# Optimization experiments

Hardware: AMD Instinct MI355X
Metric: run time of the kernel (lower is better)

## Reference

```python
import jax, jax.numpy as jnp
import numpy as np

B, T, D = 2, 4096, 512
H, W = 8, 32
HD = D // H            # 64
HIDDEN = 3 * D         # SwiGLU expansion = 3
SCALE = float(np.sqrt(HD))
EPS = 1e-5


def setup_inputs() -> dict:
    key = jax.random.key(0)
    ks = jax.random.split(key, 8)
    s = 0.02  # small init for weight matrices
    return {
        "x": jax.random.normal(ks[0], (B, T, D), dtype=jnp.float32),
        "pre_g": jnp.ones((D,), jnp.float32), "pre_b": jnp.zeros((D,), jnp.float32),
        "wq": jax.random.normal(ks[1], (D, D), jnp.float32) * s,
        "wkv": jax.random.normal(ks[2], (D, 2 * D), jnp.float32) * s,
        "wo": jax.random.normal(ks[3], (D, D), jnp.float32) * s,
        "attn_g": jnp.ones((D,), jnp.float32), "attn_b": jnp.zeros((D,), jnp.float32),
        "freqs": jax.random.normal(ks[4], (D,), jnp.float32) * 0.02,
        "phases": jnp.zeros((D,), jnp.float32),
        "amp": jnp.full((1,), 0.1, jnp.float32),
        "w_gate": jax.random.normal(ks[5], (D, HIDDEN), jnp.float32) * s,
        "w_val": jax.random.normal(ks[6], (D, HIDDEN), jnp.float32) * s,
        "w_proj": jax.random.normal(ks[7], (HIDDEN, D), jnp.float32) * s,
        "ffn_g": jnp.ones((D,), jnp.float32), "ffn_b": jnp.zeros((D,), jnp.float32),
    }


def _ln(x, g, b):
    mu = jnp.mean(x, axis=-1, keepdims=True)
    var = jnp.mean(jnp.square(x - mu), axis=-1, keepdims=True)
    return (x - mu) * jax.lax.rsqrt(var + EPS) * g + b


def _gather_window(z):
    # z: (B, T, H, C) -> nb: (B, T, W, H, C) with nb[:, t, w] = z[:, t-1-w] (zeros if t-1-w < 0)
    zp = jnp.pad(z, ((0, 0), (W, 0), (0, 0), (0, 0)))
    idx = jnp.arange(T)[:, None] + (W - 1) - jnp.arange(W)[None, :]  # (T, W), values in [0, T+W-1)
    return zp[:, idx]  # (B, T, W, H, C)


def reference(x, pre_g, pre_b, wq, wkv, wo, attn_g, attn_b,
              freqs, phases, amp, w_gate, w_val, w_proj, ffn_g, ffn_b):
    h = _ln(x, pre_g, pre_b)

    # ---- multi-head causal tension (sigmoid local attention) ----
    q = (h @ wq).reshape(B, T, H, HD)
    kv = (h @ wkv).reshape(B, T, H, 2 * HD)
    nb_kv = _gather_window(kv)                     # (B, T, W, H, 2*HD)
    nb_k, nb_v = nb_kv[..., :HD], nb_kv[..., HD:]
    tau = jax.nn.sigmoid(jnp.einsum('bthd,btwhd->bthw', q, nb_k) / SCALE)
    msg = jnp.einsum('bthw,btwhd->bthd', tau, nb_v).reshape(B, T, D)
    h = _ln(h + msg @ wo, attn_g, attn_b)

    # ---- oscillatory modulation ----
    pos = jnp.arange(T, dtype=jnp.float32)[:, None]  # (T, 1)
    mod = jnp.sin(pos * freqs + phases)              # (T, D)
    y = h * (1.0 + amp * mod)[None]

    # ---- SwiGLU FFN ----
    z = (jax.nn.silu(y @ w_gate) * (y @ w_val)) @ w_proj
    return _ln(y + z, ffn_g, ffn_b)
```

## Files before the change

kernel.cpp:

```cpp
#include <hip/hip_runtime.h>
#include <hip/hip_bf16.h>
#include <math.h>

#define T_LEN   4096
#define D_DIM   512
#define H_NUM   8
#define HD_DIM  64
#define W_WIN   32
#define HID_DIM 1536
#define M_ROWS  8192
#define QKV_LD  1536
#define BK 64

typedef __hip_bfloat16 bf16;
typedef __bf16  bf16x8 __attribute__((ext_vector_type(8)));
typedef __bf16  bf16x4 __attribute__((ext_vector_type(4)));
typedef float   f32x4  __attribute__((ext_vector_type(4)));

#define G_AS __attribute__((address_space(1)))
#define L_AS __attribute__((address_space(3)))

#define SBAR()        __builtin_amdgcn_s_barrier()
#define SCHED_FENCE() __builtin_amdgcn_sched_barrier(0)
#define WAIT_VM(N)    asm volatile("s_waitcnt vmcnt(" #N ")" ::: "memory")
#define WAIT_LGKM0()  asm volatile("s_waitcnt lgkmcnt(0)" ::: "memory")

__device__ __forceinline__ float b2f(bf16 x) { return __bfloat162float(x); }
__device__ __forceinline__ bf16  f2b(float x){ return __float2bfloat16(x); }

__device__ __forceinline__ void gload_lds16(const bf16* g, bf16* l) {
  __builtin_amdgcn_global_load_lds((const G_AS unsigned int*)g,
                                   (L_AS unsigned int*)l, 16, 0, 0);
}

__device__ __forceinline__ float rdP(const void* p, int i, bool f32) {
  return f32 ? ((const float*)p)[i] : b2f(((const bf16*)p)[i]);
}

__device__ __forceinline__ float wave_reduce_sum(float v) {
  #pragma unroll
  for (int off = 32; off; off >>= 1) v += __shfl_xor(v, off, 64);
  return v;
}

__device__ __forceinline__ bool detect_f32(const unsigned* __restrict__ x) {
  int lane = threadIdx.x & 63;
  int votes = 0;
  #pragma unroll
  for (int i = 0; i < 4; ++i) {
    unsigned e = (x[lane * 4 + i] >> 7) & 0xffu;
    votes += (e >= 90u && e <= 140u) ? 1 : 0;
  }
  float v = wave_reduce_sum((float)votes);
  return v < 200.f;
}

__device__ __forceinline__ void swizzle_xy(int gx, int& bx, int& by) {
  int lid = blockIdx.x;
  int sub = lid & 7;
  int grp = lid >> 3;
  bx = grp % gx;
  by = (grp / gx) * 8 + sub;
}

__global__ __launch_bounds__(256) void ln_kernel(
    const void* __restrict__ in, const void* __restrict__ g, const void* __restrict__ bb,
    void* __restrict__ out, int mode,
    const void* __restrict__ freqs, const void* __restrict__ phases,
    const void* __restrict__ amp,
    const unsigned* __restrict__ xdet, int in_follows, int out_follows)
{
  bool f32  = detect_f32(xdet);
  bool inF  = f32 && (in_follows != 0);
  bool outF = f32 && (out_follows != 0);

  int wave = threadIdx.x >> 6;
  int lane = threadIdx.x & 63;
  int row  = blockIdx.x * 4 + wave;

  float x[8];
  if (inF) {
    const float* rp = (const float*)in + (size_t)row * D_DIM + lane * 8;
    float4 v0 = *reinterpret_cast<const float4*>(rp);
    float4 v1 = *reinterpret_cast<const float4*>(rp + 4);
    x[0]=v0.x; x[1]=v0.y; x[2]=v0.z; x[3]=v0.w;
    x[4]=v1.x; x[5]=v1.y; x[6]=v1.z; x[7]=v1.w;
  } else {
    bf16x8 v = *reinterpret_cast<const bf16x8*>(
        (const bf16*)in + (size_t)row * D_DIM + lane * 8);
    #pragma unroll
    for (int i = 0; i < 8; ++i) x[i] = (float)v[i];
  }

  float s = 0.f, s2 = 0.f;
  #pragma unroll
  for (int i = 0; i < 8; ++i) { s += x[i]; s2 += x[i]*x[i]; }
  s  = wave_reduce_sum(s);
  s2 = wave_reduce_sum(s2);
  float mu   = s * (1.f / D_DIM);
  float var  = s2 * (1.f / D_DIM) - mu * mu;
  float rstd = rsqrtf(var + 1e-5f);

  int t = row & (T_LEN - 1);
  float ampf = (mode == 1) ? rdP(amp, 0, f32) : 0.f;

  float o[8];
  #pragma unroll
  for (int i = 0; i < 8; ++i) {
    int d = lane * 8 + i;
    float val = (x[i] - mu) * rstd * rdP(g, d, f32) + rdP(bb, d, f32);
    if (mode == 1) {
      float m = __sinf(fmaf((float)t, rdP(freqs, d, f32), rdP(phases, d, f32)));
      val *= (1.f + ampf * m);
    }
    o[i] = val;
  }

  if (outF) {
    float* op = (float*)out + (size_t)row * D_DIM + lane * 8;
    *reinterpret_cast<float4*>(op)     = make_float4(o[0], o[1], o[2], o[3]);
    *reinterpret_cast<float4*>(op + 4) = make_float4(o[4], o[5], o[6], o[7]);
  } else {
    bf16x8 ov;
    #pragma unroll
    for (int i = 0; i < 8; ++i) ov[i] = (__bf16)o[i];
    *reinterpret_cast<bf16x8*>((bf16*)out + (size_t)row * D_DIM + lane * 8) = ov;
  }
}

__global__ __launch_bounds__(256) void prep_kernel(
    const void* s0, const void* s1, const void* s2, const void* s3,
    const void* s4, const void* s5,
    bf16* d0, bf16* d1, bf16* d2, bf16* d3, bf16* d4, bf16* d5,
    const void* __restrict__ xin, const void* __restrict__ pre_g,
    const void* __restrict__ pre_b, bf16* __restrict__ hout,
    const unsigned* __restrict__ xdet)
{
  __shared__ float ftile[32][33];
  bool f32 = detect_f32(xdet);
  int bid = blockIdx.x;

  if (bid >= 3328) {
    int wave = threadIdx.x >> 6;
    int lane = threadIdx.x & 63;
    int row  = (bid - 3328) * 4 + wave;

    float x[8];
    if (f32) {
      const float* rp = (const float*)xin + (size_t)row * D_DIM + lane * 8;
      float4 v0 = *reinterpret_cast<const float4*>(rp);
      float4 v1 = *reinterpret_cast<const float4*>(rp + 4);
      x[0]=v0.x; x[1]=v0.y; x[2]=v0.z; x[3]=v0.w;
      x[4]=v1.x; x[5]=v1.y; x[6]=v1.z; x[7]=v1.w;
    } else {
      bf16x8 v = *reinterpret_cast<const bf16x8*>(
          (const bf16*)xin + (size_t)row * D_DIM + lane * 8);
      #pragma unroll
      for (int i = 0; i < 8; ++i) x[i] = (float)v[i];
    }

    float s = 0.f, s2 = 0.f;
    #pragma unroll
    for (int i = 0; i < 8; ++i) { s += x[i]; s2 += x[i]*x[i]; }
    s  = wave_reduce_sum(s);
    s2 = wave_reduce_sum(s2);
    float mu   = s * (1.f / D_DIM);
    float var  = s2 * (1.f / D_DIM) - mu * mu;
    float rstd = rsqrtf(var + 1e-5f);

    bf16x8 ov;
    #pragma unroll
    for (int i = 0; i < 8; ++i) {
      int d = lane * 8 + i;
      ov[i] = (__bf16)((x[i] - mu) * rstd * rdP(pre_g, d, f32) + rdP(pre_b, d, f32));
    }
    *reinterpret_cast<bf16x8*>(hout + (size_t)row * D_DIM + lane * 8) = ov;
    return;
  }

  const void* src; bf16* dst; int R, C, lid, tiles_x;
  if      (bid < 256)  { src=s0; dst=d0; R=512;  C=512;  lid=bid;      tiles_x=16; }
  else if (bid < 768)  { src=s1; dst=d1; R=512;  C=1024; lid=bid-256;  tiles_x=32; }
  else if (bid < 1024) { src=s2; dst=d2; R=512;  C=512;  lid=bid-768;  tiles_x=16; }
  else if (bid < 1792) { src=s3; dst=d3; R=512;  C=1536; lid=bid-1024; tiles_x=48; }
  else if (bid < 2560) { src=s4; dst=d4; R=512;  C=1536; lid=bid-1792; tiles_x=48; }
  else                 { src=s5; dst=d5; R=1536; C=512;  lid=bid-2560; tiles_x=16; }

  int c0 = (lid % tiles_x) * 32;
  int r0 = (lid / tiles_x) * 32;

  {
    int row = threadIdx.x >> 3;
    int c4  = (threadIdx.x & 7) * 4;
    if (f32) {
      float4 v = *reinterpret_cast<const float4*>(
          (const float*)src + (size_t)(r0 + row) * C + c0 + c4);
      ftile[row][c4]     = v.x;
      ftile[row][c4 + 1] = v.y;
      ftile[row][c4 + 2] = v.z;
      ftile[row][c4 + 3] = v.w;
    } else {
      bf16x4 v = *reinterpret_cast<const bf16x4*>(
          (const bf16*)src + (size_t)(r0 + row) * C + c0 + c4);
      #pragma unroll
      for (int i = 0; i < 4; ++i) ftile[row][c4 + i] = (float)v[i];
    }
  }
  __syncthreads();
  {
    int c  = threadIdx.x >> 3;
    int r4 = (threadIdx.x & 7) * 4;
    bf16x4 ov;
    #pragma unroll
    for (int i = 0; i < 4; ++i) ov[i] = (__bf16)ftile[r4 + i][c];
    *reinterpret_cast<bf16x4*>(dst + (size_t)(c0 + c) * R + r0 + r4) = ov;
  }
}

template<int BNT, bool DBUF>
__global__ __launch_bounds__(512) void gemm_tile_kernel(
    const bf16* __restrict__ A, const bf16* __restrict__ Bt,
    bf16* Cout, const bf16* extra, int N, int K, int lda, int mode, int gx)
{
  constexpr int MI  = (BNT == 128) ? 4 : 2;
  constexpr int NJ  = 2;
  constexpr int NB  = DBUF ? 2 : 1;
  constexpr int ASZ = 128 * BK;
  constexpr int BSZ = BNT * BK;
  constexpr int CPF = 68;
  constexpr int CPB = 136;
  constexpr size_t STAGE = (size_t)NB * (ASZ + BSZ) * 2;
  constexpr size_t CTSZ  = (BNT == 64) ? (size_t)128 * CPF * 4 : (size_t)128 * CPB * 2;
  constexpr size_t SMEMSZ = STAGE > CTSZ ? STAGE : CTSZ;
  __shared__ alignas(16) char smem[SMEMSZ];
  bf16* Asb = (bf16*)smem;
  bf16* Bsb = Asb + (size_t)NB * ASZ;

  int bx, by; swizzle_xy(gx, bx, by);
  int mbase = by * 128, nbase = bx * BNT;
  int tid  = threadIdx.x;
  int lane = tid & 63;
  int wid  = tid >> 6;
  int quad = lane >> 4, l16 = lane & 15;
  int wm, wn;
  if constexpr (BNT == 128) { wm = (wid >> 2) * 64; wn = (wid & 3) * 32; }
  else                      { wm = (wid >> 1) * 32; wn = (wid & 1) * 32; }

  int srow  = tid >> 3;
  int scolb = ((tid & 7) ^ (srow & 7)) * 8;
  const bf16* Ag = A  + (size_t)(mbase + srow) * lda + scolb;
  const bf16* Bg = Bt + (size_t)(nbase + srow) * K   + scolb;

  f32x4 acc[MI][NJ] = {};
  int nk = K / BK;

  auto stage = [&](int buf) {
    gload_lds16(Ag,                    &Asb[buf * ASZ + tid * 8]);
    gload_lds16(Ag + (size_t)64 * lda, &Asb[buf * ASZ + tid * 8 + 4096]);
    if constexpr (BNT == 128) {
      gload_lds16(Bg,                  &Bsb[buf * BSZ + tid * 8]);
      gload_lds16(Bg + (size_t)64 * K, &Bsb[buf * BSZ + tid * 8 + 4096]);
    } else {
      gload_lds16(Bg,                  &Bsb[buf * BSZ + tid * 8]);
    }
    Ag += BK; Bg += BK;
  };

  auto compute = [&](int cb) {
    #pragma unroll
    for (int ko = 0; ko < 2; ++ko) {
      bf16x8 a[MI], b[NJ];
      int c = ((ko * 4 + quad) ^ (l16 & 7)) * 8;
      #pragma unroll
      for (int i = 0; i < MI; ++i)
        a[i] = *reinterpret_cast<const bf16x8*>(&Asb[cb * ASZ + (wm + i * 16 + l16) * BK + c]);
      #pragma unroll
      for (int j = 0; j < NJ; ++j)
        b[j] = *reinterpret_cast<const bf16x8*>(&Bsb[cb * BSZ + (wn + j * 16 + l16) * BK + c]);
      #pragma unroll
      for (int i = 0; i < MI; ++i)
        #pragma unroll
        for (int j = 0; j < NJ; ++j)
          acc[i][j] = __builtin_amdgcn_mfma_f32_16x16x32_bf16(a[i], b[j], acc[i][j], 0, 0, 0);
    }
  };

  if constexpr (DBUF) {
    stage(0);
    for (int t = 0; t < nk; ++t) {
      int cur = t & 1;
      if (t + 1 < nk) {
        stage(cur ^ 1);
        if constexpr (BNT == 128) { WAIT_VM(4); } else { WAIT_VM(3); }
      } else {
        WAIT_VM(0);
      }
      SBAR();
      SCHED_FENCE();

      compute(cur);

      WAIT_LGKM0();
      SBAR();
      SCHED_FENCE();
    }
  } else {
    for (int t = 0; t < nk; ++t) {
      __syncthreads();
      stage(0);
      __syncthreads();
      compute(0);
    }
    __syncthreads();
  }

  if constexpr (BNT == 64) {
    float* CT = (float*)smem;
    #pragma unroll
    for (int i = 0; i < MI; ++i)
      #pragma unroll
      for (int j = 0; j < NJ; ++j)
        #pragma unroll
        for (int r = 0; r < 4; ++r)
          CT[(wm + i * 16 + quad * 4 + r) * CPF + wn + j * 16 + l16] = acc[i][j][r];
    __syncthreads();
    #pragma unroll
    for (int p = 0; p < 2; ++p) {
      int row = (tid >> 3) + p * 64;
      int c8  = tid & 7;
      const float* rp = &CT[row * CPF + c8 * 8];
      float4 v0 = *reinterpret_cast<const float4*>(rp);
      float4 v1 = *reinterpret_cast<const float4*>(rp + 4);
      float vv[8] = {v0.x, v0.y, v0.z, v0.w, v1.x, v1.y, v1.z, v1.w};
      size_t gidx = (size_t)(mbase + row) * N + nbase + c8 * 8;
      if (mode == 1) {
        bf16x8 e = *reinterpret_cast<const bf16x8*>(extra + gidx);
        #pragma unroll
        for (int k2 = 0; k2 < 8; ++k2) vv[k2] += (float)e[k2];
      }
      bf16x8 ov;
      #pragma unroll
      for (int k2 = 0; k2 < 8; ++k2) ov[k2] = (__bf16)vv[k2];
      *reinterpret_cast<bf16x8*>(Cout + gidx) = ov;
    }
  } else {
    bf16* CT = (bf16*)smem;
    #pragma unroll
    for (int i = 0; i < MI; ++i)
      #pragma unroll
      for (int j = 0; j < NJ; ++j)
        #pragma unroll
        for (int r = 0; r < 4; ++r)
          CT[(wm + i * 16 + quad * 4 + r) * CPB + wn + j * 16 + l16] = f2b(acc[i][j][r]);
    __syncthreads();
    #pragma unroll
    for (int p = 0; p < 4; ++p) {
      int row = (tid >> 4) + p * 32;
      int c16 = tid & 15;
      bf16x8 ov = *reinterpret_cast<const bf16x8*>(&CT[row * CPB + c16 * 8]);
      *reinterpret_cast<bf16x8*>(Cout + (size_t)(mbase + row) * N + nbase + c16 * 8) = ov;
    }
  }
}

__global__ __launch_bounds__(512) void gateval_kernel(
    const bf16* __restrict__ A, const bf16* __restrict__ Btg,
    const bf16* __restrict__ Btv, bf16* __restrict__ Cout,
    int N, int K, int lda, int gx)
{
  constexpr int CP = 72;
  __shared__ alignas(16) char smem[2 * (16384 + 8192 + 8192)];
  bf16* Asb = (bf16*)smem;
  bf16* Bgs = Asb + 2 * 8192;
  bf16* Bvs = Bgs + 2 * 4096;

  int bx, by; swizzle_xy(gx, bx, by);
  int mbase = by * 128, nbase = bx * 64;
  int tid  = threadIdx.x;
  int lane = tid & 63;
  int wid  = tid >> 6;
  int quad = lane >> 4, l16 = lane & 15;
  int wm = (wid >> 1) * 32, wn = (wid & 1) * 32;

  int srow  = tid >> 3;
  int scolb = ((tid & 7) ^ (srow & 7)) * 8;
  const bf16* Ag = A   + (size_t)(mbase + srow) * lda + scolb;
  const bf16* Gg = Btg + (size_t)(nbase + srow) * K   + scolb;
  const bf16* Vg = Btv + (size_t)(nbase + srow) * K   + scolb;

  f32x4 accg[2][2] = {};
  f32x4 accv[2][2] = {};
  int nk = K / BK;

  auto stage = [&](int buf) {
    gload_lds16(Ag,                    &Asb[buf * 8192 + tid * 8]);
    gload_lds16(Ag + (size_t)64 * lda, &Asb[buf * 8192 + tid * 8 + 4096]);
    gload_lds16(Gg,                    &Bgs[buf * 4096 + tid * 8]);
    gload_lds16(Vg,                    &Bvs[buf * 4096 + tid * 8]);
    Ag += BK; Gg += BK; Vg += BK;
  };

  stage(0);
  for (int t = 0; t < nk; ++t) {
    int cur = t & 1;
    if (t + 1 < nk) {
      stage(cur ^ 1);
      WAIT_VM(4);
    } else {
      WAIT_VM(0);
    }
    SBAR();
    SCHED_FENCE();

    #pragma unroll
    for (int ko = 0; ko < 2; ++ko) {
      bf16x8 a[2], bg[2], bv[2];
      int c = ((ko * 4 + quad) ^ (l16 & 7)) * 8;
      #pragma unroll
      for (int i = 0; i < 2; ++i)
        a[i]  = *reinterpret_cast<const bf16x8*>(&Asb[cur * 8192 + (wm + i * 16 + l16) * BK + c]);
      #pragma unroll
      for (int j = 0; j < 2; ++j) {
        bg[j] = *reinterpret_cast<const bf16x8*>(&Bgs[cur * 4096 + (wn + j * 16 + l16) * BK + c]);
        bv[j] = *reinterpret_cast<const bf16x8*>(&Bvs[cur * 4096 + (wn + j * 16 + l16) * BK + c]);
      }
      #pragma unroll
      for (int i = 0; i < 2; ++i)
        #pragma unroll
        for (int j = 0; j < 2; ++j) {
          accg[i][j] = __builtin_amdgcn_mfma_f32_16x16x32_bf16(a[i], bg[j], accg[i][j], 0, 0, 0);
          accv[i][j] = __builtin_amdgcn_mfma_f32_16x16x32_bf16(a[i], bv[j], accv[i][j], 0, 0, 0);
        }
    }

    WAIT_LGKM0();
    SBAR();
    SCHED_FENCE();
  }

  bf16* CT = (bf16*)smem;
  #pragma unroll
  for (int i = 0; i < 2; ++i)
    #pragma unroll
    for (int j = 0; j < 2; ++j)
      #pragma unroll
      for (int r = 0; r < 4; ++r) {
        float g = accg[i][j][r];
        float v = accv[i][j][r];
        CT[(wm + i * 16 + quad * 4 + r) * CP + wn + j * 16 + l16] =
            f2b(g / (1.f + __expf(-g)) * v);
      }
  __syncthreads();
  #pragma unroll
  for (int p = 0; p < 2; ++p) {
    int row = (tid >> 3) + p * 64;
    int c8  = tid & 7;
    bf16x8 ov = *reinterpret_cast<const bf16x8*>(&CT[row * CP + c8 * 8]);
    *reinterpret_cast<bf16x8*>(Cout + (size_t)(mbase + row) * N + nbase + c8 * 8) = ov;
  }
}

#define VT_BYTES 9216
#define PL_BYTES 2304
#define ATTN_SET (VT_BYTES + PL_BYTES)
__device__ __forceinline__ int vt_addr(int d, int t) { return d * 144 + t * 2; }

__global__ __launch_bounds__(256) void attn_mfma_kernel(bf16* qkv)
{
  __shared__ alignas(16) char lds_raw[4 * ATTN_SET];
  int lane = threadIdx.x & 63;
  int widx = threadIdx.x >> 6;
  int u    = blockIdx.x * 4 + widx;
  int tile = u >> 3, head = u & 7;
  int rowbase = tile * 16;
  int t0   = rowbase & (T_LEN - 1);
  int l16  = lane & 15, quad = lane >> 4;

  char* wbase = lds_raw + widx * ATTN_SET;
  char* Vl = wbase;
  bf16* Pl = (bf16*)(wbase + VT_BYTES);

  #pragma unroll
  for (int it = 0; it < 6; ++it) {
    int chunk = it * 64 + lane;
    int t  = chunk >> 3;
    int dc = chunk & 7;
    int row = rowbase - 32 + t;
    if (row < 0) row = 0;
    bf16x8 v = *reinterpret_cast<const bf16x8*>(
        qkv + (size_t)row * QKV_LD + 512 + head * 128 + 64 + dc * 8);
    #pragma unroll
    for (int jj = 0; jj < 8; ++jj)
      *(bf16*)(Vl + vt_addr(dc * 8 + jj, t)) = (bf16)(__bf16)v[jj];
  }
  bf16x8 z = {};
  *reinterpret_cast<bf16x8*>(Vl + vt_addr(lane, 48)) = z;
  *reinterpret_cast<bf16x8*>(Vl + vt_addr(lane, 56)) = z;

  bf16x8 aq0, aq1;
  {
    const bf16* qrow = qkv + (size_t)(rowbase + l16) * QKV_LD + head * HD_DIM + quad * 8;
    aq0 = *reinterpret_cast<const bf16x8*>(qrow);
    aq1 = *reinterpret_cast<const bf16x8*>(qrow + 32);
  }

  f32x4 sacc[3] = {};
  #pragma unroll
  for (int jt = 0; jt < 3; ++jt) {
    int tok = rowbase - 32 + jt * 16 + l16;
    if (tok < 0) tok = 0;
    const bf16* krow = qkv + (size_t)tok * QKV_LD + 512 + head * 128 + quad * 8;
    bf16x8 b0 = *reinterpret_cast<const bf16x8*>(krow);
    bf16x8 b1 = *reinterpret_cast<const bf16x8*>(krow + 32);
    sacc[jt] = __builtin_amdgcn_mfma_f32_16x16x32_bf16(aq0, b0, sacc[jt], 0, 0, 0);
    sacc[jt] = __builtin_amdgcn_mfma_f32_16x16x32_bf16(aq1, b1, sacc[jt], 0, 0, 0);
  }

  #pragma unroll
  for (int jt = 0; jt < 3; ++jt) {
    int j = jt * 16 + l16;
    #pragma unroll
    for (int r = 0; r < 4; ++r) {
      int i = quad * 4 + r;
      bool valid = (j >= i) && (j <= i + 31) && (t0 - 32 + j >= 0);
      float tau = valid ? 1.f / (1.f + __expf(-sacc[jt][r] * 0.125f)) : 0.f;
      Pl[i * 72 + j] = f2b(tau);
    }
  }
  #pragma unroll
  for (int r = 0; r < 4; ++r) Pl[(quad * 4 + r) * 72 + 48 + l16] = f2b(0.f);

  __syncthreads();

  bf16x8 ap0 = *reinterpret_cast<const bf16x8*>((char*)Pl + l16 * 144 + quad * 16);
  bf16x8 ap1 = *reinterpret_cast<const bf16x8*>((char*)Pl + l16 * 144 + 64 + quad * 16);

  f32x4 macc[4] = {};
  #pragma unroll
  for (int nt = 0; nt < 4; ++nt) {
    int d = nt * 16 + l16;
    bf16x8 bv0 = *reinterpret_cast<const bf16x8*>(Vl + vt_addr(d, quad * 8));
    bf16x8 bv1 = *reinterpret_cast<const bf16x8*>(Vl + vt_addr(d, 32 + quad * 8));
    macc[nt] = __builtin_amdgcn_mfma_f32_16x16x32_bf16(ap0, bv0, macc[nt], 0, 0, 0);
    macc[nt] = __builtin_amdgcn_mfma_f32_16x16x32_bf16(ap1, bv1, macc[nt], 0, 0, 0);
  }

  #pragma unroll
  for (int nt = 0; nt < 4; ++nt)
    #pragma unroll
    for (int r = 0; r < 4; ++r)
      Pl[(quad * 4 + r) * 72 + nt * 16 + l16] = f2b(macc[nt][r]);

  #pragma unroll
  for (int p = 0; p < 2; ++p) {
    int row = (lane >> 3) + p * 8;
    int c8  = lane & 7;
    bf16x8 ov = *reinterpret_cast<const bf16x8*>(&Pl[row * 72 + c8 * 8]);
    *reinterpret_cast<bf16x8*>(
        qkv + (size_t)(rowbase + row) * QKV_LD + head * HD_DIM + c8 * 8) = ov;
  }
}

extern "C" void kernel_launch(void* const* d_in, const int* in_sizes, int n_in,
                              void* d_out, int out_size, void* d_ws, size_t ws_size,
                              hipStream_t stream)
{
  const void* x      = d_in[0];
  const void* pre_g  = d_in[1];
  const void* pre_b  = d_in[2];
  const void* wq     = d_in[3];
  const void* wkv    = d_in[4];
  const void* wo     = d_in[5];
  const void* attn_g = d_in[6];
  const void* attn_b = d_in[7];
  const void* freqs  = d_in[8];
  const void* phases = d_in[9];
  const void* amp    = d_in[10];
  const void* w_gate = d_in[11];
  const void* w_val  = d_in[12];
  const void* w_proj = d_in[13];
  const void* ffn_g  = d_in[14];
  const void* ffn_b  = d_in[15];
  const unsigned* xdet = (const unsigned*)x;

  char* ws = (char*)d_ws;
  bf16* Btqkv = (bf16*)(ws + 512);
  bf16* Bto   = (bf16*)(ws + 1573376);
  bf16* Btg   = (bf16*)(ws + 2097664);
  bf16* Btv   = (bf16*)(ws + 3670528);
  bf16* Btp   = (bf16*)(ws + 5243392);
  bf16* h     = (bf16*)(ws + 6816256);
  bf16* qkvb  = (bf16*)(ws + 15204864);
  bf16* gb    = qkvb;

  prep_kernel<<<5376, 256, 0, stream>>>(
      wq, wkv, wo, w_gate, w_val, w_proj,
      Btqkv, Btqkv + 512 * 512, Bto, Btg, Btv, Btp,
      x, pre_g, pre_b, h, xdet);

  gemm_tile_kernel<128, false><<<768, 512, 0, stream>>>(h, Btqkv, qkvb, nullptr,
                                                        1536, 512, 512, 0, 12);

  attn_mfma_kernel<<<1024, 256, 0, stream>>>(qkvb);

  gemm_tile_kernel<64, true><<<512, 512, 0, stream>>>(qkvb, Bto, h, h,
                                                      512, 512, QKV_LD, 1, 8);

  ln_kernel<<<2048, 256, 0, stream>>>(h, attn_g, attn_b, h, 1,
                                      freqs, phases, amp, xdet, 0, 0);

  gateval_kernel<<<1536, 512, 0, stream>>>(h, Btg, Btv, gb,
                                           1536, 512, 512, 24);

  gemm_tile_kernel<64, true><<<512, 512, 0, stream>>>(gb, Btp, h, h,
                                                      512, 1536, QKV_LD, 1, 8);

  ln_kernel<<<2048, 256, 0, stream>>>(h, ffn_g, ffn_b, d_out, 0,
                                      nullptr, nullptr, nullptr, xdet, 0, 1);
}
```

Measured before the change: 259.4 us.

## Widen gate/value GEMM tile to 128x128 and drop double buffering

The fused SwiGLU gate/value GEMM now uses 128x128 output tiles instead of 128x64, with each warp computing a 64x32 sub-tile for both gate and value. This halves the grid and improves reuse of the A tile across more output columns. To fit the larger B tiles in LDS, the double-buffered async pipeline is replaced by a single buffer with syncthreads around each load, which gives up the overlap of loads with MFMA work. Register pressure per thread also rises with the larger accumulators.

```diff
diff --git a/kernel.cpp b/kernel.cpp
--- a/kernel.cpp
+++ b/kernel.cpp
@@ -368,19 +368,19 @@
     const bf16* __restrict__ Btv, bf16* __restrict__ Cout,
     int N, int K, int lda, int gx)
 {
-  constexpr int CP = 72;
-  __shared__ alignas(16) char smem[2 * (16384 + 8192 + 8192)];
+  constexpr int CP = 136;
+  __shared__ alignas(16) char smem[3 * 16384];
   bf16* Asb = (bf16*)smem;
-  bf16* Bgs = Asb + 2 * 8192;
-  bf16* Bvs = Bgs + 2 * 4096;
+  bf16* Bgs = Asb + 8192;
+  bf16* Bvs = Bgs + 8192;
 
   int bx, by; swizzle_xy(gx, bx, by);
-  int mbase = by * 128, nbase = bx * 64;
+  int mbase = by * 128, nbase = bx * 128;
   int tid  = threadIdx.x;
   int lane = tid & 63;
   int wid  = tid >> 6;
   int quad = lane >> 4, l16 = lane & 15;
-  int wm = (wid >> 1) * 32, wn = (wid & 1) * 32;
+  int wm = (wid >> 2) * 64, wn = (wid & 3) * 32;
 
   int srow  = tid >> 3;
   int scolb = ((tid & 7) ^ (srow & 7)) * 8;
@@ -388,59 +388,47 @@
   const bf16* Gg = Btg + (size_t)(nbase + srow) * K   + scolb;
   const bf16* Vg = Btv + (size_t)(nbase + srow) * K   + scolb;
 
-  f32x4 accg[2][2] = {};
-  f32x4 accv[2][2] = {};
+  f32x4 accg[4][2] = {};
+  f32x4 accv[4][2] = {};
   int nk = K / BK;
 
-  auto stage = [&](int buf) {
-    gload_lds16(Ag,                    &Asb[buf * 8192 + tid * 8]);
-    gload_lds16(Ag + (size_t)64 * lda, &Asb[buf * 8192 + tid * 8 + 4096]);
-    gload_lds16(Gg,                    &Bgs[buf * 4096 + tid * 8]);
-    gload_lds16(Vg,                    &Bvs[buf * 4096 + tid * 8]);
+  for (int t = 0; t < nk; ++t) {
+    __syncthreads();
+    gload_lds16(Ag,                    &Asb[tid * 8]);
+    gload_lds16(Ag + (size_t)64 * lda, &Asb[tid * 8 + 4096]);
+    gload_lds16(Gg,                    &Bgs[tid * 8]);
+    gload_lds16(Gg + (size_t)64 * K,   &Bgs[tid * 8 + 4096]);
+    gload_lds16(Vg,                    &Bvs[tid * 8]);
+    gload_lds16(Vg + (size_t)64 * K,   &Bvs[tid * 8 + 4096]);
     Ag += BK; Gg += BK; Vg += BK;
-  };
-
-  stage(0);
-  for (int t = 0; t < nk; ++t) {
-    int cur = t & 1;
-    if (t + 1 < nk) {
-      stage(cur ^ 1);
-      WAIT_VM(4);
-    } else {
-      WAIT_VM(0);
-    }
-    SBAR();
-    SCHED_FENCE();
+    __syncthreads();
 
     #pragma unroll
     for (int ko = 0; ko < 2; ++ko) {
-      bf16x8 a[2], bg[2], bv[2];
+      bf16x8 a[4], bg[2], bv[2];
       int c = ((ko * 4 + quad) ^ (l16 & 7)) * 8;
       #pragma unroll
-      for (int i = 0; i < 2; ++i)
-        a[i]  = *reinterpret_cast<const bf16x8*>(&Asb[cur * 8192 + (wm + i * 16 + l16) * BK + c]);
+      for (int i = 0; i < 4; ++i)
+        a[i]  = *reinterpret_cast<const bf16x8*>(&Asb[(wm + i * 16 + l16) * BK + c]);
       #pragma unroll
       for (int j = 0; j < 2; ++j) {
-        bg[j] = *reinterpret_cast<const bf16x8*>(&Bgs[cur * 4096 + (wn + j * 16 + l16) * BK + c]);
-        bv[j] = *reinterpret_cast<const bf16x8*>(&Bvs[cur * 4096 + (wn + j * 16 + l16) * BK + c]);
+        bg[j] = *reinterpret_cast<const bf16x8*>(&Bgs[(wn + j * 16 + l16) * BK + c]);
+        bv[j] = *reinterpret_cast<const bf16x8*>(&Bvs[(wn + j * 16 + l16) * BK + c]);
       }
       #pragma unroll
-      for (int i = 0; i < 2; ++i)
+      for (int i = 0; i < 4; ++i)
         #pragma unroll
         for (int j = 0; j < 2; ++j) {
           accg[i][j] = __builtin_amdgcn_mfma_f32_16x16x32_bf16(a[i], bg[j], accg[i][j], 0, 0, 0);
           accv[i][j] = __builtin_amdgcn_mfma_f32_16x16x32_bf16(a[i], bv[j], accv[i][j], 0, 0, 0);
         }
     }
-
-    WAIT_LGKM0();
-    SBAR();
-    SCHED_FENCE();
-  }
+  }
+  __syncthreads();
 
   bf16* CT = (bf16*)smem;
   #pragma unroll
-  for (int i = 0; i < 2; ++i)
+  for (int i = 0; i < 4; ++i)
     #pragma unroll
     for (int j = 0; j < 2; ++j)
       #pragma unroll
@@ -452,11 +440,11 @@
       }
   __syncthreads();
   #pragma unroll
-  for (int p = 0; p < 2; ++p) {
-    int row = (tid >> 3) + p * 64;
-    int c8  = tid & 7;
-    bf16x8 ov = *reinterpret_cast<const bf16x8*>(&CT[row * CP + c8 * 8]);
-    *reinterpret_cast<bf16x8*>(Cout + (size_t)(mbase + row) * N + nbase + c8 * 8) = ov;
+  for (int p = 0; p < 4; ++p) {
+    int row = (tid >> 4) + p * 32;
+    int c16 = tid & 15;
+    bf16x8 ov = *reinterpret_cast<const bf16x8*>(&CT[row * CP + c16 * 8]);
+    *reinterpret_cast<bf16x8*>(Cout + (size_t)(mbase + row) * N + nbase + c16 * 8) = ov;
   }
 }
 
@@ -609,8 +597,8 @@
   ln_kernel<<<2048, 256, 0, stream>>>(h, attn_g, attn_b, h, 1,
                                       freqs, phases, amp, xdet, 0, 0);
 
-  gateval_kernel<<<1536, 512, 0, stream>>>(h, Btg, Btv, gb,
-                                           1536, 512, 512, 24);
+  gateval_kernel<<<768, 512, 0, stream>>>(h, Btg, Btv, gb,
+                                          1536, 512, 512, 12);
 
   gemm_tile_kernel<64, true><<<512, 512, 0, stream>>>(gb, Btp, h, h,
                                                       512, 1536, QKV_LD, 1, 8);
```

Result: no change. 262.9 us (+1.4%).
